# Kernel tuning notes

Hardware: AMD Instinct MI355X
Metric: run time of the kernel (lower is better)

Reference implementation:

```python
import jax, jax.numpy as jnp
import numpy as np

B = 131072   # batch rows in the (pooled) sparse tensor
C = 512      # conv_out4
J = 7        # jnt_dim
H = 512      # linear_out
TAU_MAX = 1.0  # undefined global in source; torque cap, taken as 1.0
EPS = 1e-5


def layer_norm(x, g, b):
    m = jnp.mean(x, axis=-1, keepdims=True)
    v = jnp.var(x, axis=-1, keepdims=True)
    return (x - m) * jax.lax.rsqrt(v + EPS) * g + b


def setup_inputs() -> dict:
    key = jax.random.key(0)
    ks = jax.random.split(key, 6)
    return {
        "features": jax.random.normal(ks[0], (B, C), dtype=jnp.float32),
        "coords": jax.random.randint(ks[1], (B,), 0, B),  # batch indices (col 0 of ME coords)
        "jnt_pos": jax.random.normal(ks[2], (B, J), dtype=jnp.float32),
        "jnt_goal": jax.random.normal(ks[3], (B, J), dtype=jnp.float32),
        "ln1_g": jnp.ones((C,), jnp.float32),
        "ln1_b": jnp.zeros((C,), jnp.float32),
        "W1": jax.random.normal(ks[4], (C + 2 * J, H), dtype=jnp.float32) / np.sqrt(C + 2 * J),
        "b1": jnp.zeros((H,), jnp.float32),
        "ln2_g": jnp.ones((H,), jnp.float32),
        "ln2_b": jnp.zeros((H,), jnp.float32),
        "W2": jax.random.normal(ks[5], (H, J), dtype=jnp.float32) / np.sqrt(H),
        "b2": jnp.zeros((J,), jnp.float32),
    }


def reference(features, coords, jnt_pos, jnt_goal,
              ln1_g, ln1_b, W1, b1, ln2_g, ln2_b, W2, b2):
    # to_dense_tnsr: y = zeros_like(features); for c in coords: y[c] = features[c]
    # vectorized: single gather + scatter (duplicate writes carry identical values)
    y = jnp.zeros_like(features).at[coords].set(features[coords])
    # norm = LayerNorm(512) -> SELU   (dropout in eval mode: identity)
    x = jax.nn.selu(layer_norm(y, ln1_g, ln1_b))
    # cat((jnt_pos, jnt_goal, x), dim=1)
    x = jnp.concatenate([jnt_pos, jnt_goal, x], axis=1)  # [B, 2J+C]
    # linear = Linear -> LayerNorm -> SELU
    x = jax.nn.selu(layer_norm(x @ W1 + b1, ln2_g, ln2_b))
    # out = Linear -> Tanh, scaled by tau_max
    return jnp.tanh(x @ W2 + b2) * TAU_MAX
```

## Files before the change

kernel.cpp:

```cpp
#include <hip/hip_runtime.h>

#define B_ROWS   131072
#define MTILE    64
#define KCHUNKS  17
#define LDA      552
#define LDX      528
#define W1F_OFF  ((size_t)B_ROWS)
#define W2F_OFF  (W1F_OFF + (size_t)544 * 512 * 2)
#define X1_OFF   (W2F_OFF + (size_t)16 * 512 * 2)
#define X1_BYTES ((size_t)B_ROWS * LDA * 2)

typedef _Float16 f16x8 __attribute__((ext_vector_type(8)));
typedef float    f32x4 __attribute__((ext_vector_type(4)));
typedef float    fv4   __attribute__((ext_vector_type(4)));
typedef unsigned int uv2 __attribute__((ext_vector_type(2)));

__device__ inline unsigned short f2h(float f) {
  _Float16 h = (_Float16)f;
  return __builtin_bit_cast(unsigned short, h);
}
__device__ inline float selu_f(float x) {
  const float lam = 1.0507009873554805f, alp = 1.6732632423543772f;
  return x > 0.f ? lam * x : lam * alp * (__expf(x) - 1.f);
}
__device__ inline void gld16nt(const void* g, void* l) {
  __builtin_amdgcn_global_load_lds(
      (const __attribute__((address_space(1))) unsigned int*)g,
      (__attribute__((address_space(3))) unsigned int*)l, 16, 0, 2);
}

__global__ void scatter_mask(const int* __restrict__ coords,
                             unsigned char* __restrict__ mask) {
  int i = blockIdx.x * 256 + threadIdx.x;
  mask[coords[i]] = 1u;
}

__global__ void build_wf(const float* __restrict__ W1, const float* __restrict__ W2,
                         unsigned short* __restrict__ W1f, unsigned short* __restrict__ W2f) {
  int tid = threadIdx.x;
  if (blockIdx.x < 544) {
    int fragIdx = blockIdx.x;
    int ni = fragIdx & 3;
    int c  = (fragIdx >> 2) % 17;
    int wq = fragIdx / 68;
    int nbase = wq * 64 + ni * 16;
    __shared__ float t[32][17];
    int kl = tid >> 4, nl = tid & 15;
    int kg = c * 32 + kl;
    float v = 0.f;
    if (kg < 512)      v = W1[(size_t)(kg + 14) * 512 + nbase + nl];
    else if (kg < 526) v = W1[(size_t)(kg - 512) * 512 + nbase + nl];
    t[kl][nl] = v;
    __syncthreads();
    int lane = tid >> 3, e = tid & 7;
    int k2 = ((lane >> 4) & 3) * 8 + e;
    int n2 = lane & 15;
    W1f[(size_t)fragIdx * 512 + tid] = f2h(t[k2][n2]);
  } else {
    int c2 = blockIdx.x - 544;
    int lane = tid >> 3, e = tid & 7;
    int n = lane & 15, quad = (lane >> 4) & 3;
    int k = c2 * 32 + quad * 8 + e;
    float v = (n < 7) ? W2[(size_t)k * 7 + n] : 0.f;
    W2f[(size_t)c2 * 512 + tid] = f2h(v);
  }
}

__global__ __launch_bounds__(512) void ln1_kernel(
    const float* __restrict__ feat, const unsigned char* __restrict__ mask,
    const float* __restrict__ jp, const float* __restrict__ jg,
    const float* __restrict__ ln1g, const float* __restrict__ ln1b,
    unsigned short* __restrict__ X1) {
  const int w = threadIdx.x >> 6, lane = threadIdx.x & 63;
  const size_t row = (size_t)blockIdx.x * 8 + w;
  float mk = mask[row] ? 1.f : 0.f;
  const fv4* frow = (const fv4*)feat + row * 128;
  fv4 f0 = __builtin_nontemporal_load(frow + lane);
  fv4 f1 = __builtin_nontemporal_load(frow + 64 + lane);
  float s = f0.x + f0.y + f0.z + f0.w + f1.x + f1.y + f1.z + f1.w;
  float q = f0.x * f0.x + f0.y * f0.y + f0.z * f0.z + f0.w * f0.w +
            f1.x * f1.x + f1.y * f1.y + f1.z * f1.z + f1.w * f1.w;
#pragma unroll
  for (int d = 32; d > 0; d >>= 1) { s += __shfl_xor(s, d); q += __shfl_xor(q, d); }
  float mean = mk * s * (1.f / 512.f);
  float msq  = mk * q * (1.f / 512.f);
  float rstd = rsqrtf(msq - mean * mean + 1e-5f);
  unsigned short* xr = X1 + row * LDA;
  {
    float4 g = ((const float4*)ln1g)[lane], b = ((const float4*)ln1b)[lane];
    union { unsigned short us[4]; uv2 u; } pk;
    pk.us[0] = f2h(selu_f((f0.x * mk - mean) * rstd * g.x + b.x));
    pk.us[1] = f2h(selu_f((f0.y * mk - mean) * rstd * g.y + b.y));
    pk.us[2] = f2h(selu_f((f0.z * mk - mean) * rstd * g.z + b.z));
    pk.us[3] = f2h(selu_f((f0.w * mk - mean) * rstd * g.w + b.w));
    __builtin_nontemporal_store(pk.u, (uv2*)&xr[lane * 4]);
  }
  {
    float4 g = ((const float4*)ln1g)[64 + lane], b = ((const float4*)ln1b)[64 + lane];
    union { unsigned short us[4]; uv2 u; } pk;
    pk.us[0] = f2h(selu_f((f1.x * mk - mean) * rstd * g.x + b.x));
    pk.us[1] = f2h(selu_f((f1.y * mk - mean) * rstd * g.y + b.y));
    pk.us[2] = f2h(selu_f((f1.z * mk - mean) * rstd * g.z + b.z));
    pk.us[3] = f2h(selu_f((f1.w * mk - mean) * rstd * g.w + b.w));
    __builtin_nontemporal_store(pk.u, (uv2*)&xr[256 + lane * 4]);
  }
  if (lane < 16) {
    int kk = 2 * lane;
    float v0 = 0.f, v1 = 0.f;
    if (kk < 7)       v0 = jp[row * 7 + kk];
    else if (kk < 14) v0 = jg[row * 7 + kk - 7];
    if (kk + 1 < 7)       v1 = jp[row * 7 + kk + 1];
    else if (kk + 1 < 14) v1 = jg[row * 7 + kk - 6];
    union { unsigned short us[2]; unsigned int u; } pj;
    pj.us[0] = f2h(v0); pj.us[1] = f2h(v1);
    __builtin_nontemporal_store(pj.u, (unsigned int*)&xr[512 + 2 * lane]);
  } else if (lane < 20) {
    __builtin_nontemporal_store(0u, (unsigned int*)&xr[544 + 2 * (lane - 16)]);
  }
}

struct __align__(16) SMemG {
  char buf[70656];
  float part[8][MTILE][2];
  float mean2[MTILE], rstd2[MTILE];
};

__global__ __launch_bounds__(512, 4) void actor_gemm(
    const unsigned short* __restrict__ X1,
    const unsigned short* __restrict__ W1f, const float* __restrict__ b1,
    const float* __restrict__ ln2g, const float* __restrict__ ln2b,
    const unsigned short* __restrict__ W2f, const float* __restrict__ b2,
    float* __restrict__ out) {
  __shared__ SMemG sm;
  unsigned short* At = (unsigned short*)sm.buf;
  unsigned short* X2 = (unsigned short*)sm.buf;
  float*          O  = (float*)(sm.buf + 64 * LDX * 2);

  const int tid  = threadIdx.x;
  const int wq   = tid >> 6;
  const int lane = tid & 63;
  const int m0   = blockIdx.x * MTILE;
  const int mrow = lane & 15;
  const int quad = lane >> 4;

  {
    const char* src = (const char*)X1 + (size_t)m0 * (LDA * 2);
#pragma unroll
    for (int i = 0; i < 8; ++i) {
      int chunk = i * 8 + wq;
      gld16nt(src + (size_t)chunk * 1024 + lane * 16, (char*)sm.buf + chunk * 1024);
    }
    if (wq < 5) {
      int chunk = 64 + wq;
      gld16nt(src + (size_t)chunk * 1024 + lane * 16, (char*)sm.buf + chunk * 1024);
    }
  }

  const unsigned short* wBase = W1f + (size_t)wq * 68 * 512 + lane * 8;
  f16x8 bE[4], bO[4];
#pragma unroll
  for (int ni = 0; ni < 4; ++ni)
    bE[ni] = *(const f16x8*)(wBase + (size_t)ni * 512);

  __syncthreads();

  f32x4 acc[4][4];
#pragma unroll
  for (int mi = 0; mi < 4; ++mi)
#pragma unroll
    for (int ni = 0; ni < 4; ++ni) acc[mi][ni] = (f32x4){0.f, 0.f, 0.f, 0.f};

  const unsigned short* aB = At + mrow * LDA + quad * 8;

  auto loadB = [&](f16x8* dst, int c) {
#pragma unroll
    for (int ni = 0; ni < 4; ++ni)
      dst[ni] = *(const f16x8*)(wBase + (size_t)(c * 4 + ni) * 512);
  };
  auto step = [&](const f16x8* bF, int c) {
    f16x8 a[4];
#pragma unroll
    for (int mi = 0; mi < 4; ++mi)
      a[mi] = *(const f16x8*)(aB + mi * 16 * LDA + c * 32);
#pragma unroll
    for (int mi = 0; mi < 4; ++mi)
#pragma unroll
      for (int ni = 0; ni < 4; ++ni)
        acc[mi][ni] = __builtin_amdgcn_mfma_f32_16x16x32_f16(a[mi], bF[ni], acc[mi][ni], 0, 0, 0);
  };

  for (int c = 0; c < KCHUNKS - 1; c += 2) {
    loadB(bO, c + 1);
    step(bE, c);
    loadB(bE, c + 2);
    step(bO, c + 1);
  }
  step(bE, 16);

  f16x8 bW2[2];
  bW2[0] = *(const f16x8*)&W2f[(size_t)(2 * wq)     * 512 + lane * 8];
  bW2[1] = *(const f16x8*)&W2f[(size_t)(2 * wq + 1) * 512 + lane * 8];

  float b1v[4], g2v[4], bl2v[4];
#pragma unroll
  for (int ni = 0; ni < 4; ++ni) {
    int col = wq * 64 + ni * 16 + mrow;
    b1v[ni] = b1[col]; g2v[ni] = ln2g[col]; bl2v[ni] = ln2b[col];
  }
#pragma unroll
  for (int mi = 0; mi < 4; ++mi)
#pragma unroll
    for (int reg = 0; reg < 4; ++reg) {
      int r = mi * 16 + quad * 4 + reg;
      float s = 0.f, q = 0.f;
#pragma unroll
      for (int ni = 0; ni < 4; ++ni) {
        float v = acc[mi][ni][reg] + b1v[ni];
        acc[mi][ni][reg] = v;
        s += v; q += v * v;
      }
      s += __shfl_xor(s, 1); q += __shfl_xor(q, 1);
      s += __shfl_xor(s, 2); q += __shfl_xor(q, 2);
      s += __shfl_xor(s, 4); q += __shfl_xor(q, 4);
      s += __shfl_xor(s, 8); q += __shfl_xor(q, 8);
      if ((lane & 15) == 0) { sm.part[wq][r][0] = s; sm.part[wq][r][1] = q; }
    }
  __syncthreads();
  if (tid < MTILE) {
    float s = 0.f, q = 0.f;
#pragma unroll
    for (int w = 0; w < 8; ++w) { s += sm.part[w][tid][0]; q += sm.part[w][tid][1]; }
    float mean = s * (1.f / 512.f);
    float var  = q * (1.f / 512.f) - mean * mean;
    sm.mean2[tid] = mean;
    sm.rstd2[tid] = rsqrtf(var + 1e-5f);
  }
  O[tid] = 0.f;
  __syncthreads();
#pragma unroll
  for (int mi = 0; mi < 4; ++mi)
#pragma unroll
    for (int ni = 0; ni < 4; ++ni)
#pragma unroll
      for (int reg = 0; reg < 4; ++reg) {
        int r = mi * 16 + quad * 4 + reg;
        int col = wq * 64 + ni * 16 + mrow;
        float v = (acc[mi][ni][reg] - sm.mean2[r]) * sm.rstd2[r] * g2v[ni] + bl2v[ni];
        X2[r * LDX + col] = f2h(selu_f(v));
      }
  __syncthreads();

  {
    f32x4 acc2[4];
#pragma unroll
    for (int mi = 0; mi < 4; ++mi) acc2[mi] = (f32x4){0.f, 0.f, 0.f, 0.f};
#pragma unroll
    for (int j = 0; j < 2; ++j) {
      int c2 = 2 * wq + j;
#pragma unroll
      for (int mi = 0; mi < 4; ++mi) {
        f16x8 a = *(const f16x8*)&X2[(mi * 16 + mrow) * LDX + c2 * 32 + quad * 8];
        acc2[mi] = __builtin_amdgcn_mfma_f32_16x16x32_f16(a, bW2[j], acc2[mi], 0, 0, 0);
      }
    }
#pragma unroll
    for (int mi = 0; mi < 4; ++mi)
#pragma unroll
      for (int reg = 0; reg < 4; ++reg)
        if (mrow < 7)
          atomicAdd(&O[(mi * 16 + quad * 4 + reg) * 8 + mrow], acc2[mi][reg]);
  }
  __syncthreads();
  {
    int r = tid >> 3, c = tid & 7;
    if (c < 7)
      out[(size_t)(m0 + r) * 7 + c] = tanhf(O[tid] + b2[c]);
  }
}

struct __align__(16) SMemF {
  char buf[70656];
  float rsum[MTILE], rsq[MTILE], mean2[MTILE], rstd2[MTILE];
};

__global__ __launch_bounds__(512, 4) void actor_fused(
    const float* __restrict__ feat, const unsigned char* __restrict__ mask,
    const float* __restrict__ jp, const float* __restrict__ jg,
    const float* __restrict__ ln1g, const float* __restrict__ ln1b,
    const unsigned short* __restrict__ W1f, const float* __restrict__ b1,
    const float* __restrict__ ln2g, const float* __restrict__ ln2b,
    const unsigned short* __restrict__ W2f, const float* __restrict__ b2,
    float* __restrict__ out) {
  __shared__ SMemF sm;
  unsigned short* At = (unsigned short*)sm.buf;
  unsigned short* X2 = (unsigned short*)sm.buf;
  float*          O  = (float*)(sm.buf + 64 * LDX * 2);

  const int tid  = threadIdx.x;
  const int wq   = tid >> 6;
  const int lane = tid & 63;
  const int m0   = blockIdx.x * MTILE;
  const int mrow = lane & 15;
  const int quad = lane >> 4;

  if (tid < MTILE) { sm.rsum[tid] = 0.f; sm.rsq[tid] = 0.f; }

  const unsigned short* wBase = W1f + (size_t)wq * 68 * 512 + lane * 8;
  f16x8 bE[4], bO[4];
#pragma unroll
  for (int ni = 0; ni < 4; ++ni)
    bE[ni] = *(const f16x8*)(wBase + (size_t)ni * 512);

  {
    const int arow = tid >> 3;
    const int acg  = tid & 7;
    const int row  = m0 + arow;
    const float4* frow = (const float4*)feat + (size_t)row * 128 + acg;
    float4 f[16];
    float s = 0.f, q = 0.f;
#pragma unroll
    for (int c = 0; c < 16; ++c) {
      float4 v = frow[(size_t)c * 8];
      f[c] = v;
      s += v.x + v.y + v.z + v.w;
      q += v.x * v.x + v.y * v.y + v.z * v.z + v.w * v.w;
    }
    s += __shfl_xor(s, 1); q += __shfl_xor(q, 1);
    s += __shfl_xor(s, 2); q += __shfl_xor(q, 2);
    s += __shfl_xor(s, 4); q += __shfl_xor(q, 4);
    float mk   = mask[row] ? 1.f : 0.f;
    float mean = mk * s * (1.f / 512.f);
    float msq  = mk * q * (1.f / 512.f);
    float rstd = rsqrtf(msq - mean * mean + 1e-5f);
#pragma unroll
    for (int c = 0; c < 16; ++c) {
      float4 g = ((const float4*)ln1g)[c * 8 + acg];
      float4 b = ((const float4*)ln1b)[c * 8 + acg];
      union { unsigned short us[4]; uint2 u; } pk;
      pk.us[0] = f2h(selu_f((f[c].x * mk - mean) * rstd * g.x + b.x));
      pk.us[1] = f2h(selu_f((f[c].y * mk - mean) * rstd * g.y + b.y));
      pk.us[2] = f2h(selu_f((f[c].z * mk - mean) * rstd * g.z + b.z));
      pk.us[3] = f2h(selu_f((f[c].w * mk - mean) * rstd * g.w + b.w));
      *(uint2*)&At[arow * LDA + c * 32 + acg * 4] = pk.u;
    }
    {
      union { unsigned short us[4]; uint2 u; } pk;
#pragma unroll
      for (int q2 = 0; q2 < 4; ++q2) {
        int kk = acg * 4 + q2;
        float val = 0.f;
        if (kk < 7)       val = jp[(size_t)row * 7 + kk];
        else if (kk < 14) val = jg[(size_t)row * 7 + kk - 7];
        pk.us[q2] = f2h(val);
      }
      *(uint2*)&At[arow * LDA + 512 + acg * 4] = pk.u;
    }
  }
  __syncthreads();

  f32x4 acc[4][4];
#pragma unroll
  for (int mi = 0; mi < 4; ++mi)
#pragma unroll
    for (int ni = 0; ni < 4; ++ni) acc[mi][ni] = (f32x4){0.f, 0.f, 0.f, 0.f};

  const unsigned short* aB = At + mrow * LDA + quad * 8;
  auto loadB = [&](f16x8* dst, int c) {
#pragma unroll
    for (int ni = 0; ni < 4; ++ni)
      dst[ni] = *(const f16x8*)(wBase + (size_t)(c * 4 + ni) * 512);
  };
  auto step = [&](const f16x8* bF, int c) {
    f16x8 a[4];
#pragma unroll
    for (int mi = 0; mi < 4; ++mi)
      a[mi] = *(const f16x8*)(aB + mi * 16 * LDA + c * 32);
#pragma unroll
    for (int mi = 0; mi < 4; ++mi)
#pragma unroll
      for (int ni = 0; ni < 4; ++ni)
        acc[mi][ni] = __builtin_amdgcn_mfma_f32_16x16x32_f16(a[mi], bF[ni], acc[mi][ni], 0, 0, 0);
  };
  for (int c = 0; c < KCHUNKS - 1; c += 2) {
    loadB(bO, c + 1);
    step(bE, c);
    loadB(bE, c + 2);
    step(bO, c + 1);
  }
  step(bE, 16);

  f16x8 bW2[2];
  bW2[0] = *(const f16x8*)&W2f[(size_t)(2 * wq)     * 512 + lane * 8];
  bW2[1] = *(const f16x8*)&W2f[(size_t)(2 * wq + 1) * 512 + lane * 8];

  float b1v[4], g2v[4], bl2v[4];
#pragma unroll
  for (int ni = 0; ni < 4; ++ni) {
    int col = wq * 64 + ni * 16 + mrow;
    b1v[ni] = b1[col]; g2v[ni] = ln2g[col]; bl2v[ni] = ln2b[col];
  }
#pragma unroll
  for (int mi = 0; mi < 4; ++mi)
#pragma unroll
    for (int reg = 0; reg < 4; ++reg) {
      int r = mi * 16 + quad * 4 + reg;
      float s = 0.f, q = 0.f;
#pragma unroll
      for (int ni = 0; ni < 4; ++ni) {
        float v = acc[mi][ni][reg] + b1v[ni];
        acc[mi][ni][reg] = v;
        s += v; q += v * v;
      }
      s += __shfl_xor(s, 1); q += __shfl_xor(q, 1);
      s += __shfl_xor(s, 2); q += __shfl_xor(q, 2);
      s += __shfl_xor(s, 4); q += __shfl_xor(q, 4);
      s += __shfl_xor(s, 8); q += __shfl_xor(q, 8);
      if ((lane & 15) == 0) { atomicAdd(&sm.rsum[r], s); atomicAdd(&sm.rsq[r], q); }
    }
  __syncthreads();
  if (tid < MTILE) {
    float mean = sm.rsum[tid] * (1.f / 512.f);
    float var  = sm.rsq[tid] * (1.f / 512.f) - mean * mean;
    sm.mean2[tid] = mean;
    sm.rstd2[tid] = rsqrtf(var + 1e-5f);
  }
  O[tid] = 0.f;
  __syncthreads();
#pragma unroll
  for (int mi = 0; mi < 4; ++mi)
#pragma unroll
    for (int ni = 0; ni < 4; ++ni)
#pragma unroll
      for (int reg = 0; reg < 4; ++reg) {
        int r = mi * 16 + quad * 4 + reg;
        int col = wq * 64 + ni * 16 + mrow;
        float v = (acc[mi][ni][reg] - sm.mean2[r]) * sm.rstd2[r] * g2v[ni] + bl2v[ni];
        X2[r * LDX + col] = f2h(selu_f(v));
      }
  __syncthreads();
  {
    f32x4 acc2[4];
#pragma unroll
    for (int mi = 0; mi < 4; ++mi) acc2[mi] = (f32x4){0.f, 0.f, 0.f, 0.f};
#pragma unroll
    for (int j = 0; j < 2; ++j) {
      int c2 = 2 * wq + j;
#pragma unroll
      for (int mi = 0; mi < 4; ++mi) {
        f16x8 a = *(const f16x8*)&X2[(mi * 16 + mrow) * LDX + c2 * 32 + quad * 8];
        acc2[mi] = __builtin_amdgcn_mfma_f32_16x16x32_f16(a, bW2[j], acc2[mi], 0, 0, 0);
      }
    }
#pragma unroll
    for (int mi = 0; mi < 4; ++mi)
#pragma unroll
      for (int reg = 0; reg < 4; ++reg)
        if (mrow < 7)
          atomicAdd(&O[(mi * 16 + quad * 4 + reg) * 8 + mrow], acc2[mi][reg]);
  }
  __syncthreads();
  {
    int r = tid >> 3, c = tid & 7;
    if (c < 7)
      out[(size_t)(m0 + r) * 7 + c] = tanhf(O[tid] + b2[c]);
  }
}

extern "C" void kernel_launch(void* const* d_in, const int* in_sizes, int n_in,
                              void* d_out, int out_size, void* d_ws, size_t ws_size,
                              hipStream_t stream) {
  const float* feat  = (const float*)d_in[0];
  const int*   crd   = (const int*)d_in[1];
  const float* jp    = (const float*)d_in[2];
  const float* jg    = (const float*)d_in[3];
  const float* ln1g  = (const float*)d_in[4];
  const float* ln1b  = (const float*)d_in[5];
  const float* W1    = (const float*)d_in[6];
  const float* b1    = (const float*)d_in[7];
  const float* ln2g  = (const float*)d_in[8];
  const float* ln2b  = (const float*)d_in[9];
  const float* W2    = (const float*)d_in[10];
  const float* b2    = (const float*)d_in[11];
  float* out = (float*)d_out;

  unsigned char*  mask = (unsigned char*)d_ws;
  unsigned short* W1f  = (unsigned short*)((char*)d_ws + W1F_OFF);
  unsigned short* W2f  = (unsigned short*)((char*)d_ws + W2F_OFF);
  unsigned short* X1   = (unsigned short*)((char*)d_ws + X1_OFF);

  (void)hipMemsetAsync(mask, 0, (size_t)B_ROWS, stream);
  scatter_mask<<<B_ROWS / 256, 256, 0, stream>>>(crd, mask);
  build_wf<<<560, 512, 0, stream>>>(W1, W2, W1f, W2f);

  if (ws_size >= X1_OFF + X1_BYTES) {
    ln1_kernel<<<B_ROWS / 8, 512, 0, stream>>>(feat, mask, jp, jg, ln1g, ln1b, X1);
    actor_gemm<<<B_ROWS / MTILE, 512, 0, stream>>>(
        X1, W1f, b1, ln2g, ln2b, W2f, b2, out);
  } else {
    actor_fused<<<B_ROWS / MTILE, 512, 0, stream>>>(
        feat, mask, jp, jg, ln1g, ln1b, W1f, b1, ln2g, ln2b, W2f, b2, out);
  }
}
```

Before: 543.4 us.

## Double actor_gemm row tile to 128 rows per block for W1 reuse

The GEMM kernel now handles 128 rows per block instead of 64. Each W1 fragment loaded from global memory is reused across twice as many MFMA row tiles, which halves total W1 traffic. In exchange it uses about 141 KB of LDS and 128 accumulator registers per lane for the first GEMM, occupancy bounds drop from 4 to 2 blocks, and the epilogue writes twice as many outputs.

```diff
diff --git a/kernel.cpp b/kernel.cpp
--- a/kernel.cpp
+++ b/kernel.cpp
@@ -2,6 +2,7 @@
 
 #define B_ROWS   131072
 #define MTILE    64
+#define MT2      128
 #define KCHUNKS  17
 #define LDA      552
 #define LDX      528
@@ -120,12 +121,12 @@
 }
 
 struct __align__(16) SMemG {
-  char buf[70656];
-  float part[8][MTILE][2];
-  float mean2[MTILE], rstd2[MTILE];
+  char buf[141312];
+  float part[8][MT2][2];
+  float mean2[MT2], rstd2[MT2];
 };
 
-__global__ __launch_bounds__(512, 4) void actor_gemm(
+__global__ __launch_bounds__(512, 2) void actor_gemm(
     const unsigned short* __restrict__ X1,
     const unsigned short* __restrict__ W1f, const float* __restrict__ b1,
     const float* __restrict__ ln2g, const float* __restrict__ ln2b,
@@ -134,24 +135,24 @@
   __shared__ SMemG sm;
   unsigned short* At = (unsigned short*)sm.buf;
   unsigned short* X2 = (unsigned short*)sm.buf;
-  float*          O  = (float*)(sm.buf + 64 * LDX * 2);
+  float*          O  = (float*)(sm.buf + MT2 * LDX * 2);
 
   const int tid  = threadIdx.x;
   const int wq   = tid >> 6;
   const int lane = tid & 63;
-  const int m0   = blockIdx.x * MTILE;
+  const int m0   = blockIdx.x * MT2;
   const int mrow = lane & 15;
   const int quad = lane >> 4;
 
   {
     const char* src = (const char*)X1 + (size_t)m0 * (LDA * 2);
 #pragma unroll
-    for (int i = 0; i < 8; ++i) {
+    for (int i = 0; i < 17; ++i) {
       int chunk = i * 8 + wq;
       gld16nt(src + (size_t)chunk * 1024 + lane * 16, (char*)sm.buf + chunk * 1024);
     }
-    if (wq < 5) {
-      int chunk = 64 + wq;
+    if (wq < 2) {
+      int chunk = 136 + wq;
       gld16nt(src + (size_t)chunk * 1024 + lane * 16, (char*)sm.buf + chunk * 1024);
     }
   }
@@ -164,9 +165,9 @@
 
   __syncthreads();
 
-  f32x4 acc[4][4];
-#pragma unroll
-  for (int mi = 0; mi < 4; ++mi)
+  f32x4 acc[8][4];
+#pragma unroll
+  for (int mi = 0; mi < 8; ++mi)
 #pragma unroll
     for (int ni = 0; ni < 4; ++ni) acc[mi][ni] = (f32x4){0.f, 0.f, 0.f, 0.f};
 
@@ -178,15 +179,13 @@
       dst[ni] = *(const f16x8*)(wBase + (size_t)(c * 4 + ni) * 512);
   };
   auto step = [&](const f16x8* bF, int c) {
-    f16x8 a[4];
-#pragma unroll
-    for (int mi = 0; mi < 4; ++mi)
-      a[mi] = *(const f16x8*)(aB + mi * 16 * LDA + c * 32);
-#pragma unroll
-    for (int mi = 0; mi < 4; ++mi)
+#pragma unroll
+    for (int mi = 0; mi < 8; ++mi) {
+      f16x8 a = *(const f16x8*)(aB + mi * 16 * LDA + c * 32);
 #pragma unroll
       for (int ni = 0; ni < 4; ++ni)
-        acc[mi][ni] = __builtin_amdgcn_mfma_f32_16x16x32_f16(a[mi], bF[ni], acc[mi][ni], 0, 0, 0);
+        acc[mi][ni] = __builtin_amdgcn_mfma_f32_16x16x32_f16(a, bF[ni], acc[mi][ni], 0, 0, 0);
+    }
   };
 
   for (int c = 0; c < KCHUNKS - 1; c += 2) {
@@ -208,7 +207,7 @@
     b1v[ni] = b1[col]; g2v[ni] = ln2g[col]; bl2v[ni] = ln2b[col];
   }
 #pragma unroll
-  for (int mi = 0; mi < 4; ++mi)
+  for (int mi = 0; mi < 8; ++mi)
 #pragma unroll
     for (int reg = 0; reg < 4; ++reg) {
       int r = mi * 16 + quad * 4 + reg;
@@ -226,7 +225,7 @@
       if ((lane & 15) == 0) { sm.part[wq][r][0] = s; sm.part[wq][r][1] = q; }
     }
   __syncthreads();
-  if (tid < MTILE) {
+  if (tid < MT2) {
     float s = 0.f, q = 0.f;
 #pragma unroll
     for (int w = 0; w < 8; ++w) { s += sm.part[w][tid][0]; q += sm.part[w][tid][1]; }
@@ -235,10 +234,10 @@
     sm.mean2[tid] = mean;
     sm.rstd2[tid] = rsqrtf(var + 1e-5f);
   }
-  O[tid] = 0.f;
-  __syncthreads();
-#pragma unroll
-  for (int mi = 0; mi < 4; ++mi)
+  O[tid] = 0.f; O[512 + tid] = 0.f;
+  __syncthreads();
+#pragma unroll
+  for (int mi = 0; mi < 8; ++mi)
 #pragma unroll
     for (int ni = 0; ni < 4; ++ni)
 #pragma unroll
@@ -251,30 +250,32 @@
   __syncthreads();
 
   {
-    f32x4 acc2[4];
-#pragma unroll
-    for (int mi = 0; mi < 4; ++mi) acc2[mi] = (f32x4){0.f, 0.f, 0.f, 0.f};
+    f32x4 acc2[8];
+#pragma unroll
+    for (int mi = 0; mi < 8; ++mi) acc2[mi] = (f32x4){0.f, 0.f, 0.f, 0.f};
 #pragma unroll
     for (int j = 0; j < 2; ++j) {
       int c2 = 2 * wq + j;
 #pragma unroll
-      for (int mi = 0; mi < 4; ++mi) {
+      for (int mi = 0; mi < 8; ++mi) {
         f16x8 a = *(const f16x8*)&X2[(mi * 16 + mrow) * LDX + c2 * 32 + quad * 8];
         acc2[mi] = __builtin_amdgcn_mfma_f32_16x16x32_f16(a, bW2[j], acc2[mi], 0, 0, 0);
       }
     }
 #pragma unroll
-    for (int mi = 0; mi < 4; ++mi)
+    for (int mi = 0; mi < 8; ++mi)
 #pragma unroll
       for (int reg = 0; reg < 4; ++reg)
         if (mrow < 7)
           atomicAdd(&O[(mi * 16 + quad * 4 + reg) * 8 + mrow], acc2[mi][reg]);
   }
   __syncthreads();
-  {
-    int r = tid >> 3, c = tid & 7;
+#pragma unroll
+  for (int it = 0; it < 2; ++it) {
+    int idx = it * 512 + tid;
+    int r = idx >> 3, c = idx & 7;
     if (c < 7)
-      out[(size_t)(m0 + r) * 7 + c] = tanhf(O[tid] + b2[c]);
+      out[(size_t)(m0 + r) * 7 + c] = tanhf(O[idx] + b2[c]);
   }
 }
 
@@ -494,7 +495,7 @@
 
   if (ws_size >= X1_OFF + X1_BYTES) {
     ln1_kernel<<<B_ROWS / 8, 512, 0, stream>>>(feat, mask, jp, jg, ln1g, ln1b, X1);
-    actor_gemm<<<B_ROWS / MTILE, 512, 0, stream>>>(
+    actor_gemm<<<B_ROWS / MT2, 512, 0, stream>>>(
         X1, W1f, b1, ln2g, ln2b, W2f, b2, out);
   } else {
     actor_fused<<<B_ROWS / MTILE, 512, 0, stream>>>(
```

Measured after the change: 556.4 us. 1.02x slower.
